# Kernel optimization log

Hardware: AMD Instinct MI355X
Metric: run time of the kernel (lower is better)

Reference implementation:

```python
import jax, jax.numpy as jnp
import numpy as np

N, E = 50000, 800000
HID, HEADS, HD = 128, 4, 32
EDIM, EGD = 16, 32


def _ln(x, g, b):
    mu = jnp.mean(x, axis=-1, keepdims=True)
    var = jnp.mean((x - mu) ** 2, axis=-1, keepdims=True)
    return (x - mu) / jnp.sqrt(var + 1e-5) * g + b


def _gelu(z):
    return jax.nn.gelu(z, approximate=False)


def setup_inputs() -> dict:
    key = jax.random.key(0)
    ks = jax.random.split(key, 16)
    n = lambda k, shape, s=1.0: jax.random.normal(k, shape, dtype=jnp.float32) * s
    return {
        "x": n(ks[0], (N, HID)),
        "edge_index": jax.random.randint(ks[1], (2, E), 0, N, dtype=jnp.int32),
        "edge_attr": n(ks[2], (E, EDIM)),
        "gamma": jax.random.uniform(ks[3], (N, HID), dtype=jnp.float32),
        "beta": n(ks[4], (N, HID), 0.1),
        "ln1_g": jnp.ones((HID,), jnp.float32), "ln1_b": jnp.zeros((HID,), jnp.float32),
        "Wq": n(ks[5], (HID, HEADS * HD), 0.05),
        "Wk": n(ks[6], (HID, HEADS * HD), 0.05),
        "Wv": n(ks[7], (HID, HEADS * HD), 0.05),
        "Wo": n(ks[8], (HEADS * HD, HID), 0.05), "bo": jnp.zeros((HID,), jnp.float32),
        "Wea1": n(ks[9], (EDIM, EGD), 0.1), "bea1": jnp.zeros((EGD,), jnp.float32),
        "Wea2": n(ks[10], (EGD, HEADS), 0.1), "bea2": jnp.zeros((HEADS,), jnp.float32),
        "Weg1": n(ks[11], (EDIM, EGD), 0.1), "beg1": jnp.zeros((EGD,), jnp.float32),
        "Weg2": n(ks[12], (EGD, HEADS * HD), 0.1), "beg2": jnp.zeros((HEADS * HD,), jnp.float32),
        "ln2_g": jnp.ones((HID,), jnp.float32), "ln2_b": jnp.zeros((HID,), jnp.float32),
        "Wf1": n(ks[13], (HID, 2 * HID), 0.05), "bf1": jnp.zeros((2 * HID,), jnp.float32),
        "Wf2": n(ks[14], (2 * HID, HID), 0.05), "bf2": jnp.zeros((HID,), jnp.float32),
    }


def reference(x, edge_index, edge_attr, gamma, beta,
              ln1_g, ln1_b, Wq, Wk, Wv, Wo, bo,
              Wea1, bea1, Wea2, bea2, Weg1, beg1, Weg2, beg2,
              ln2_g, ln2_b, Wf1, bf1, Wf2, bf2):
    n_nodes = x.shape[0]
    src, dst = edge_index[0], edge_index[1]
    scale = HD ** -0.5

    x_n = _ln(x, ln1_g, ln1_b)
    Q = (x_n @ Wq).reshape(n_nodes, HEADS, HD)
    K = (x_n @ Wk).reshape(n_nodes, HEADS, HD)
    V = (x_n @ Wv).reshape(n_nodes, HEADS, HD)

    # per-edge attention logits, edge-bias modulated  [E, h]
    logits = jnp.einsum('ehd,ehd->eh', Q[dst], K[src]) * scale
    logits = logits + (_gelu(edge_attr @ Wea1 + bea1) @ Wea2 + bea2)

    # sparse softmax over destination neighbourhoods (torch scatter_reduce amax
    # includes the zero-initialised accumulator -> max with 0)
    m = jax.ops.segment_max(logits, dst, num_segments=n_nodes)
    m = jnp.maximum(m, 0.0)
    el = jnp.exp(logits - m[dst])
    s = jax.ops.segment_sum(el, dst, num_segments=n_nodes)
    attn = el / (s[dst] + 1e-10)                      # [E, h]

    # per-edge sigmoid gate on values  [E, h, d]
    e_gate = jax.nn.sigmoid(_gelu(edge_attr @ Weg1 + beg1) @ Weg2 + beg2)
    weighted = attn[:, :, None] * (e_gate.reshape(-1, HEADS, HD) * V[src])
    out = jax.ops.segment_sum(weighted, dst, num_segments=n_nodes)
    out = out.reshape(n_nodes, HEADS * HD) @ Wo + bo

    out = gamma * out + beta                          # FiLM (dropout=0, eval)
    x = x + out
    x = x + (_gelu(_ln(x, ln2_g, ln2_b) @ Wf1 + bf1) @ Wf2 + bf2)
    return x
```

## Files before the change

### kernel.cpp

```cpp
#include <hip/hip_runtime.h>
#include <cmath>

#define N_NODES 50000
#define E_EDGES 800000
#define HID 128
#define HEADS 4
#define EDIM 16
#define EGD 32
#define VSTRIDE 136
#define SCAN_BS 512
#define SCAN_NB ((N_NODES + SCAN_BS - 1) / SCAN_BS)

typedef __attribute__((ext_vector_type(8))) short bf16x8;
typedef __attribute__((ext_vector_type(4))) float f32x4;

__device__ __forceinline__ float erf_fast(float x) {
    const float ax = fabsf(x);
    const float t = __builtin_amdgcn_rcpf(fmaf(0.3275911f, ax, 1.0f));
    float p = fmaf(1.061405429f, t, -1.453152027f);
    p = fmaf(p, t, 1.421413741f);
    p = fmaf(p, t, -0.284496736f);
    p = fmaf(p, t, 0.254829592f);
    p = p * t;
    const float e = __expf(-ax * ax);
    const float r = fmaf(-p, e, 1.0f);
    return copysignf(r, x);
}
__device__ __forceinline__ float gelu_f(float z) {
    return 0.5f * z * (1.0f + erf_fast(z * 0.7071067811865476f));
}
__device__ __forceinline__ float sigmoid_fast(float z) {
    return __builtin_amdgcn_rcpf(1.0f + __expf(-z));
}
__device__ __forceinline__ short f2bf(float f) {
    unsigned u = __float_as_uint(f);
    unsigned r = u + 0x7fffu + ((u >> 16) & 1u);
    return (short)(r >> 16);
}
__device__ __forceinline__ float bf2f(unsigned short u) {
    return __uint_as_float(((unsigned)u) << 16);
}

__global__ void __launch_bounds__(256) k0w_conv(
    const float* __restrict__ Wq, const float* __restrict__ Wk, const float* __restrict__ Wv,
    const float* __restrict__ Wo, const float* __restrict__ Wf1, const float* __restrict__ Wf2,
    const float* __restrict__ Wea1, const float* __restrict__ Wea2,
    const float* __restrict__ Weg1, const float* __restrict__ Weg2,
    unsigned short* __restrict__ Wqm, unsigned short* __restrict__ Wkm,
    unsigned short* __restrict__ Wvm, unsigned short* __restrict__ Wom,
    unsigned short* __restrict__ Wf1m, unsigned short* __restrict__ Wf2m,
    unsigned short* __restrict__ Wea1m, unsigned short* __restrict__ Wea2m,
    unsigned short* __restrict__ Wg1m, unsigned short* __restrict__ Wg2m)
{
    const int b = blockIdx.x, t = threadIdx.x;
    if (b == 512) {
        for (int i = t; i < 1024; i += 256) {
            const int j = i & 7, rest = i >> 3;
            const int n = rest & 31, q = rest >> 5, k = q * 8 + j;
            Wea1m[i] = (unsigned short)((k < EDIM) ? f2bf(Wea1[k * EGD + n]) : (short)0);
        }
        for (int i = t; i < 512; i += 256) {
            const int j = i & 7, rest = i >> 3;
            const int n = rest & 15, q = rest >> 4, k = q * 8 + j;
            Wea2m[i] = (unsigned short)((n < HEADS) ? f2bf(Wea2[k * HEADS + n]) : (short)0);
        }
        for (int i = t; i < 1024; i += 256) {
            const int j = i & 7, rest = i >> 3;
            const int c15 = rest & 15, qn = rest >> 4;
            const int q = qn >> 1, n = qn & 1;
            const int k = q * 8 + j;
            Wg1m[i] = (unsigned short)((k < EDIM) ? f2bf(Weg1[k * EGD + n * 16 + c15]) : (short)0);
        }
        for (int i = t; i < 4096; i += 256) {
            const int j = i & 7, rest = i >> 3;
            const int c15 = rest & 15, rest2 = rest >> 4;
            const int tt = rest2 & 7, q = rest2 >> 3;
            const int k = q * 8 + j;
            Wg2m[i] = (unsigned short)f2bf(Weg2[k * HID + tt * 16 + c15]);
        }
        return;
    }
    const float* src; unsigned short* dst; int idx; bool wide;
    if (b < 64)       { src = Wq;  dst = Wqm;  idx = b * 256 + t;         wide = false; }
    else if (b < 128) { src = Wk;  dst = Wkm;  idx = (b - 64) * 256 + t;  wide = false; }
    else if (b < 192) { src = Wv;  dst = Wvm;  idx = (b - 128) * 256 + t; wide = false; }
    else if (b < 256) { src = Wo;  dst = Wom;  idx = (b - 192) * 256 + t; wide = false; }
    else if (b < 384) { src = Wf1; dst = Wf1m; idx = (b - 256) * 256 + t; wide = true;  }
    else              { src = Wf2; dst = Wf2m; idx = (b - 384) * 256 + t; wide = false; }
    int k, n, N;
    if (wide) { k = idx >> 8; n = idx & 255; N = 256; }
    else      { k = idx >> 7; n = idx & 127; N = 128; }
    dst[((size_t)(k >> 3) * N + n) * 8 + (k & 7)] = (unsigned short)f2bf(src[idx]);
}

__global__ void __launch_bounds__(256) k1_ln_qkv(
    const float* __restrict__ x, const float* __restrict__ g1, const float* __restrict__ b1,
    const unsigned short* __restrict__ Wqm, const unsigned short* __restrict__ Wkm,
    const unsigned short* __restrict__ Wvm,
    unsigned short* __restrict__ Qb, unsigned short* __restrict__ Kb,
    unsigned short* __restrict__ Vb)
{
    __shared__ float xsm[16][HID];
    __shared__ __align__(16) unsigned short xnb[16 * HID];
    const int t = threadIdx.x;
    const int base = blockIdx.x * 16;
    {
        const float4* src = (const float4*)(x + (size_t)base * HID);
        float4* dst = (float4*)xsm;
        dst[t] = src[t];
        dst[t + 256] = src[t + 256];
    }
    __syncthreads();
    {
        const int sr = t >> 4, sl = t & 15;
        float s1 = 0.f, s2 = 0.f, v[8];
        #pragma unroll
        for (int j = 0; j < 8; ++j) { v[j] = xsm[sr][sl + 16 * j]; s1 += v[j]; s2 += v[j] * v[j]; }
        #pragma unroll
        for (int m = 1; m < 16; m <<= 1) { s1 += __shfl_xor(s1, m); s2 += __shfl_xor(s2, m); }
        const float mu = s1 * (1.0f / HID);
        const float rstd = rsqrtf(s2 * (1.0f / HID) - mu * mu + 1e-5f);
        char* rowp = (char*)(xnb + sr * HID);
        #pragma unroll
        for (int j = 0; j < 8; ++j) {
            const int col = sl + 16 * j;
            const float nv = (v[j] - mu) * rstd * g1[col] + b1[col];
            *(unsigned short*)(rowp + ((col * 2) ^ ((sr & 7) << 4))) = (unsigned short)f2bf(nv);
        }
    }
    __syncthreads();
    const int w = t >> 6, l = t & 63, q = l >> 4, c15 = l & 15;
    bf16x8 a[4];
    {
        const char* rowp = (const char*)(xnb + c15 * HID);
        #pragma unroll
        for (int kc = 0; kc < 4; ++kc)
            a[kc] = *(const bf16x8*)(rowp + ((kc * 64 + q * 16) ^ ((c15 & 7) << 4)));
    }
    const f32x4 zc = {0.f, 0.f, 0.f, 0.f};
    #pragma unroll
    for (int ct = 0; ct < 2; ++ct) {
        const int colb = (w * 2 + ct) * 16;
        f32x4 aq = zc, ak = zc, av = zc;
        #pragma unroll
        for (int kc = 0; kc < 4; ++kc) {
            const size_t boff = (size_t)((kc * 4 + q) * HID + colb + c15) * 8;
            aq = __builtin_amdgcn_mfma_f32_16x16x32_bf16(a[kc], *(const bf16x8*)(Wqm + boff), aq, 0, 0, 0);
            ak = __builtin_amdgcn_mfma_f32_16x16x32_bf16(a[kc], *(const bf16x8*)(Wkm + boff), ak, 0, 0, 0);
            av = __builtin_amdgcn_mfma_f32_16x16x32_bf16(a[kc], *(const bf16x8*)(Wvm + boff), av, 0, 0, 0);
        }
        #pragma unroll
        for (int r = 0; r < 4; ++r) {
            const size_t idx = (size_t)(base + q * 4 + r) * HID + colb + c15;
            Qb[idx] = (unsigned short)f2bf(aq[r]);
            Kb[idx] = (unsigned short)f2bf(ak[r]);
            Vb[idx] = (unsigned short)f2bf(av[r]);
        }
    }
}

__global__ void __launch_bounds__(256) k0a_degree(
    const int* __restrict__ ei, int* __restrict__ deg)
{
    const int e = blockIdx.x * 256 + threadIdx.x;
    atomicAdd(deg + ei[E_EDGES + e], 1);
}

__global__ void __launch_bounds__(SCAN_BS) k0b_scan1(
    const int* __restrict__ deg, int* __restrict__ rowptr, int* __restrict__ bsum)
{
    __shared__ int sm[SCAN_BS];
    const int t = threadIdx.x;
    const int i = blockIdx.x * SCAN_BS + t;
    const int v = (i < N_NODES) ? deg[i] : 0;
    sm[t] = v;
    __syncthreads();
    #pragma unroll
    for (int off = 1; off < SCAN_BS; off <<= 1) {
        int add = (t >= off) ? sm[t - off] : 0;
        __syncthreads();
        sm[t] += add;
        __syncthreads();
    }
    if (i < N_NODES) rowptr[i] = sm[t] - v;
    if (t == SCAN_BS - 1) bsum[blockIdx.x] = sm[t];
}

__global__ void __launch_bounds__(128) k0c_scan2(int* __restrict__ bsum)
{
    __shared__ int sm[128];
    const int t = threadIdx.x;
    const int v = (t < SCAN_NB) ? bsum[t] : 0;
    sm[t] = v;
    __syncthreads();
    #pragma unroll
    for (int off = 1; off < 128; off <<= 1) {
        int add = (t >= off) ? sm[t - off] : 0;
        __syncthreads();
        sm[t] += add;
        __syncthreads();
    }
    if (t < SCAN_NB) bsum[t] = sm[t] - v;
}

__global__ void __launch_bounds__(SCAN_BS) k0d_fixup(
    int* __restrict__ rowptr, int* __restrict__ wptr, const int* __restrict__ bsum)
{
    const int i = blockIdx.x * SCAN_BS + threadIdx.x;
    if (i < N_NODES) {
        int r = rowptr[i] + bsum[blockIdx.x];
        rowptr[i] = r;
        wptr[i] = r;
    }
    if (i == 0) rowptr[N_NODES] = E_EDGES;
}

__global__ void __launch_bounds__(256) k0e_scatter(
    const int* __restrict__ ei, int* __restrict__ wptr,
    int* __restrict__ eidx, int* __restrict__ esrc, int* __restrict__ pdst)
{
    const int e = blockIdx.x * 256 + threadIdx.x;
    const int d = ei[E_EDGES + e];
    const int pos = atomicAdd(wptr + d, 1);
    eidx[pos] = e;
    esrc[pos] = ei[e];
    pdst[pos] = d;
}

__global__ void __launch_bounds__(256) k2_fused(
    const int* __restrict__ eidx, const int* __restrict__ esrc, const int* __restrict__ pdst,
    const unsigned short* __restrict__ Qb, const unsigned short* __restrict__ Kb,
    const float* __restrict__ ea,
    const unsigned short* __restrict__ Wea1m, const float* __restrict__ bea1,
    const unsigned short* __restrict__ Wea2m, const float* __restrict__ bea2,
    float* __restrict__ logits,
    unsigned short* __restrict__ eab)
{
    __shared__ __align__(16) float dot_lds[4][16][4];
    __shared__ __align__(16) short h_lds[4][16 * EGD];
    const int t = threadIdx.x;
    const int w = t >> 6, l = t & 63;
    const int p0 = blockIdx.x * 64 + w * 16;

    {
        const int er = l >> 4;
        const int i = l & 15;
        const int head = i >> 2, part = i & 3;
        #pragma unroll
        for (int cc = 0; cc < 4; ++cc) {
            const int p = p0 + cc * 4 + er;
            const int dst = pdst[p], src = esrc[p];
            const bf16x8 qv = *(const bf16x8*)(Qb + (size_t)dst * HID + head * 32 + part * 8);
            const bf16x8 kv = *(const bf16x8*)(Kb + (size_t)src * HID + head * 32 + part * 8);
            float s = 0.f;
            #pragma unroll
            for (int j = 0; j < 8; ++j)
                s = fmaf(bf2f((unsigned short)qv[j]), bf2f((unsigned short)kv[j]), s);
            s += __shfl_xor(s, 1);
            s += __shfl_xor(s, 2);
            if (part == 0) dot_lds[w][cc * 4 + er][head] = s * 0.17677669529663689f;
        }
    }

    const int q = l >> 4, c15 = l & 15;
    bf16x8 a1 = {0, 0, 0, 0, 0, 0, 0, 0};
    if (q < 2) {
        const int e = eidx[p0 + c15];
        const float4 u0 = *(const float4*)(ea + (size_t)e * EDIM + q * 8);
        const float4 u1 = *(const float4*)(ea + (size_t)e * EDIM + q * 8 + 4);
        a1[0] = f2bf(u0.x); a1[1] = f2bf(u0.y); a1[2] = f2bf(u0.z); a1[3] = f2bf(u0.w);
        a1[4] = f2bf(u1.x); a1[5] = f2bf(u1.y); a1[6] = f2bf(u1.z); a1[7] = f2bf(u1.w);
        *(bf16x8*)(eab + (size_t)(p0 + c15) * EDIM + q * 8) = a1;
    }
    const bf16x8 b1f0 = *(const bf16x8*)(Wea1m + (size_t)(q * 32 + c15) * 8);
    const bf16x8 b1f1 = *(const bf16x8*)(Wea1m + (size_t)(q * 32 + 16 + c15) * 8);
    const f32x4 zc = {0.f, 0.f, 0.f, 0.f};
    f32x4 c0 = __builtin_amdgcn_mfma_f32_16x16x32_bf16(a1, b1f0, zc, 0, 0, 0);
    f32x4 c1 = __builtin_amdgcn_mfma_f32_16x16x32_bf16(a1, b1f1, zc, 0, 0, 0);
    const float bb0 = bea1[c15], bb1 = bea1[16 + c15];
    #pragma unroll
    for (int r = 0; r < 4; ++r) {
        h_lds[w][(q * 4 + r) * EGD + c15]      = f2bf(gelu_f(c0[r] + bb0));
        h_lds[w][(q * 4 + r) * EGD + 16 + c15] = f2bf(gelu_f(c1[r] + bb1));
    }
    asm volatile("s_waitcnt lgkmcnt(0)" ::: "memory");
    __builtin_amdgcn_sched_barrier(0);
    const bf16x8 a2 = *(const bf16x8*)&h_lds[w][c15 * EGD + q * 8];
    const bf16x8 b2 = *(const bf16x8*)(Wea2m + (size_t)(q * 16 + c15) * 8);
    f32x4 d2 = __builtin_amdgcn_mfma_f32_16x16x32_bf16(a2, b2, zc, 0, 0, 0);
    if (c15 < 4) {
        const float be = bea2[c15];
        #pragma unroll
        for (int r = 0; r < 4; ++r) {
            const int edge = q * 4 + r;
            const int p = p0 + edge;
            logits[(size_t)p * 4 + c15] = dot_lds[w][edge][c15] + d2[r] + be;
        }
    }
}

__global__ void __launch_bounds__(256, 8) k4_mfma(
    const int* __restrict__ rowptr, const int* __restrict__ esrc,
    const unsigned short* __restrict__ eab,
    const unsigned short* __restrict__ Wg1m, const float* __restrict__ beg1,
    const unsigned short* __restrict__ Wg2m, const float* __restrict__ beg2,
    const float* __restrict__ logits,
    const unsigned short* __restrict__ Vb, unsigned short* __restrict__ aggb)
{
    __shared__ __align__(16) short h_lds[4][16 * EGD];
    __shared__ __align__(16) float attn_lds[4][16][4];
    __shared__ __align__(16) unsigned short vsm[4][16 * VSTRIDE];
    const int t = threadIdx.x;
    const int wid = t >> 6, l = t & 63;
    const int q = l >> 4, c15 = l & 15;

    const float b1c0 = beg1[c15], b1c1 = beg1[16 + c15];
    float bg2[8];
    #pragma unroll
    for (int tt = 0; tt < 8; ++tt) bg2[tt] = beg2[tt * 16 + c15];

    const f32x4 zc = {0.f, 0.f, 0.f, 0.f};
    const int n = blockIdx.x * 4 + wid;
    const int pstart = rowptr[n], pend = rowptr[n + 1];

    const int pidx = pstart + l;
    const int my_src = (pidx < pend) ? esrc[pidx] : 0;

    const int slot = l >> 2, head = l & 3;
    float ssum = 0.f, el0 = 0.f;
    for (int pc = pstart; pc < pend; pc += 16) {
        const int cnt = min(16, pend - pc);
        float el = 0.f;
        if (slot < cnt) el = __expf(logits[(size_t)(pc + slot) * 4 + head]);
        if (pc == pstart) el0 = el;
        ssum += el;
    }
    ssum += __shfl_xor(ssum, 4);
    ssum += __shfl_xor(ssum, 8);
    ssum += __shfl_xor(ssum, 16);
    ssum += __shfl_xor(ssum, 32);
    const float invh = __builtin_amdgcn_rcpf(ssum + 1e-10f);

    float accv[8];
    #pragma unroll
    for (int tt = 0; tt < 8; ++tt) accv[tt] = 0.f;

    const int srow = l >> 2;
    const int ssub = l & 3;

    for (int pc = pstart; pc < pend; pc += 16) {
        const int cnt = min(16, pend - pc);
        const int sidx = (srow < cnt) ? srow : cnt - 1;
        const int rel = pc - pstart + sidx;
        const int srcrow = (rel < 64) ? __shfl(my_src, rel) : esrc[pc + sidx];
        bf16x8 vreg[4];
        #pragma unroll
        for (int i = 0; i < 4; ++i)
            vreg[i] = *(const bf16x8*)(Vb + (size_t)srcrow * HID + ssub * 32 + i * 8);
        const float el = (pc == pstart) ? el0
            : ((slot < cnt) ? __expf(logits[(size_t)(pc + slot) * 4 + head]) : 0.f);
        attn_lds[wid][slot][head] = el * invh;
        bf16x8 a1 = {0, 0, 0, 0, 0, 0, 0, 0};
        if (q < 2 && c15 < cnt)
            a1 = *(const bf16x8*)(eab + (size_t)(pc + c15) * EDIM + q * 8);
        const bf16x8 b1f0 = *(const bf16x8*)(Wg1m + (size_t)((q * 2 + 0) * 16 + c15) * 8);
        const bf16x8 b1f1 = *(const bf16x8*)(Wg1m + (size_t)((q * 2 + 1) * 16 + c15) * 8);
        f32x4 c0 = __builtin_amdgcn_mfma_f32_16x16x32_bf16(a1, b1f0, zc, 0, 0, 0);
        f32x4 c1 = __builtin_amdgcn_mfma_f32_16x16x32_bf16(a1, b1f1, zc, 0, 0, 0);
        #pragma unroll
        for (int r = 0; r < 4; ++r) {
            h_lds[wid][(q * 4 + r) * EGD + c15]      = f2bf(gelu_f(c0[r] + b1c0));
            h_lds[wid][(q * 4 + r) * EGD + 16 + c15] = f2bf(gelu_f(c1[r] + b1c1));
        }
        #pragma unroll
        for (int i = 0; i < 4; ++i)
            *(bf16x8*)&vsm[wid][srow * VSTRIDE + ssub * 32 + i * 8] = vreg[i];
        asm volatile("s_waitcnt lgkmcnt(0)" ::: "memory");
        __builtin_amdgcn_sched_barrier(0);
        const bf16x8 a2 = *(const bf16x8*)&h_lds[wid][c15 * EGD + q * 8];
        f32x4 at[4];
        #pragma unroll
        for (int r = 0; r < 4; ++r)
            at[r] = *(const f32x4*)&attn_lds[wid][q * 4 + r][0];
        f32x4 g[8];
        #pragma unroll
        for (int tt = 0; tt < 8; ++tt) {
            const bf16x8 b2 = *(const bf16x8*)(Wg2m + (size_t)((q * 8 + tt) * 16 + c15) * 8);
            g[tt] = __builtin_amdgcn_mfma_f32_16x16x32_bf16(a2, b2, zc, 0, 0, 0);
        }
        #pragma unroll
        for (int tt = 0; tt < 8; ++tt) {
            #pragma unroll
            for (int r = 0; r < 4; ++r) {
                const float sg = sigmoid_fast(g[tt][r] + bg2[tt]);
                const float aw = (tt < 2) ? at[r][0] : (tt < 4) ? at[r][1]
                               : (tt < 6) ? at[r][2] : at[r][3];
                const float vv = bf2f(vsm[wid][(q * 4 + r) * VSTRIDE + tt * 16 + c15]);
                accv[tt] = fmaf(aw * sg, vv, accv[tt]);
            }
        }
    }
    #pragma unroll
    for (int tt = 0; tt < 8; ++tt) {
        accv[tt] += __shfl_xor(accv[tt], 16);
        accv[tt] += __shfl_xor(accv[tt], 32);
    }
    aggb[(size_t)n * HID + (2 * q) * 16 + c15]     = (unsigned short)f2bf(accv[2 * q]);
    aggb[(size_t)n * HID + (2 * q + 1) * 16 + c15] = (unsigned short)f2bf(accv[2 * q + 1]);
}

__global__ void __launch_bounds__(256) k5_out(
    const unsigned short* __restrict__ aggb, const unsigned short* __restrict__ Wom,
    const float* __restrict__ bo,
    const float* __restrict__ gamma, const float* __restrict__ beta,
    const float* __restrict__ x,
    const float* __restrict__ g2, const float* __restrict__ b2,
    const unsigned short* __restrict__ Wf1m, const float* __restrict__ bf1,
    const unsigned short* __restrict__ Wf2m, const float* __restrict__ bf2,
    float* __restrict__ out)
{
    __shared__ float xlsm[16][HID];
    __shared__ __align__(16) unsigned short xnb[16 * HID];
    __shared__ __align__(16) unsigned short hb[16 * 2 * HID];
    const int t = threadIdx.x;
    const int base = blockIdx.x * 16;
    const int w = t >> 6, l = t & 63, q = l >> 4, c15 = l & 15;
    const f32x4 zc = {0.f, 0.f, 0.f, 0.f};

    bf16x8 a[4];
    #pragma unroll
    for (int kc = 0; kc < 4; ++kc)
        a[kc] = *(const bf16x8*)(aggb + (size_t)(base + c15) * HID + kc * 32 + q * 8);
    float xl[2][4];
    #pragma unroll
    for (int ct = 0; ct < 2; ++ct) {
        const int colb = (w * 2 + ct) * 16;
        f32x4 acc = zc;
        #pragma unroll
        for (int kc = 0; kc < 4; ++kc)
            acc = __builtin_amdgcn_mfma_f32_16x16x32_bf16(
                a[kc], *(const bf16x8*)(Wom + (size_t)((kc * 4 + q) * HID + colb + c15) * 8), acc, 0, 0, 0);
        const float bov = bo[colb + c15];
        #pragma unroll
        for (int r = 0; r < 4; ++r) {
            const int row = q * 4 + r;
            const size_t idx = (size_t)(base + row) * HID + colb + c15;
            float o = acc[r] + bov;
            o = fmaf(gamma[idx], o, beta[idx]);
            const float v = x[idx] + o;
            xl[ct][r] = v;
            xlsm[row][colb + c15] = v;
        }
    }
    __syncthreads();
    {
        const int sr = t >> 4, sl = t & 15;
        float s1 = 0.f, s2 = 0.f, v[8];
        #pragma unroll
        for (int j = 0; j < 8; ++j) { v[j] = xlsm[sr][sl + 16 * j]; s1 += v[j]; s2 += v[j] * v[j]; }
        #pragma unroll
        for (int m = 1; m < 16; m <<= 1) { s1 += __shfl_xor(s1, m); s2 += __shfl_xor(s2, m); }
        const float mu = s1 * (1.0f / HID);
        const float rstd = rsqrtf(s2 * (1.0f / HID) - mu * mu + 1e-5f);
        char* rowp = (char*)(xnb + sr * HID);
        #pragma unroll
        for (int j = 0; j < 8; ++j) {
            const int col = sl + 16 * j;
            const float nv = (v[j] - mu) * rstd * g2[col] + b2[col];
            *(unsigned short*)(rowp + ((col * 2) ^ ((sr & 7) << 4))) = (unsigned short)f2bf(nv);
        }
    }
    __syncthreads();
    {
        const char* rowp = (const char*)(xnb + c15 * HID);
        bf16x8 a2[4];
        #pragma unroll
        for (int kc = 0; kc < 4; ++kc)
            a2[kc] = *(const bf16x8*)(rowp + ((kc * 64 + q * 16) ^ ((c15 & 7) << 4)));
        #pragma unroll
        for (int ct = 0; ct < 4; ++ct) {
            const int colb = (w * 4 + ct) * 16;
            f32x4 acc = zc;
            #pragma unroll
            for (int kc = 0; kc < 4; ++kc)
                acc = __builtin_amdgcn_mfma_f32_16x16x32_bf16(
                    a2[kc], *(const bf16x8*)(Wf1m + (size_t)((kc * 4 + q) * 256 + colb + c15) * 8), acc, 0, 0, 0);
            const float b1v = bf1[colb + c15];
            #pragma unroll
            for (int r = 0; r < 4; ++r) {
                const int row = q * 4 + r;
                const float hg = gelu_f(acc[r] + b1v);
                *(unsigned short*)((char*)(hb + row * 2 * HID)
                    + (((colb + c15) * 2) ^ ((row & 7) << 4))) = (unsigned short)f2bf(hg);
            }
        }
    }
    __syncthreads();
    {
        const char* rowp = (const char*)(hb + c15 * 2 * HID);
        bf16x8 a3[8];
        #pragma unroll
        for (int kc = 0; kc < 8; ++kc)
            a3[kc] = *(const bf16x8*)(rowp + ((kc * 64 + q * 16) ^ ((c15 & 7) << 4)));
        #pragma unroll
        for (int ct = 0; ct < 2; ++ct) {
            const int colb = (w * 2 + ct) * 16;
            f32x4 acc = zc;
            #pragma unroll
            for (int kc = 0; kc < 8; ++kc)
                acc = __builtin_amdgcn_mfma_f32_16x16x32_bf16(
                    a3[kc], *(const bf16x8*)(Wf2m + (size_t)((kc * 4 + q) * HID + colb + c15) * 8), acc, 0, 0, 0);
            const float b2v = bf2[colb + c15];
            #pragma unroll
            for (int r = 0; r < 4; ++r) {
                const int row = q * 4 + r;
                out[(size_t)(base + row) * HID + colb + c15] = xl[ct][r] + acc[r] + b2v;
            }
        }
    }
}

extern "C" void kernel_launch(void* const* d_in, const int* in_sizes, int n_in,
                              void* d_out, int out_size, void* d_ws, size_t ws_size,
                              hipStream_t stream) {
    const float* x     = (const float*)d_in[0];
    const int*   ei    = (const int*)d_in[1];
    const float* ea    = (const float*)d_in[2];
    const float* gamma = (const float*)d_in[3];
    const float* beta  = (const float*)d_in[4];
    const float* ln1_g = (const float*)d_in[5];
    const float* ln1_b = (const float*)d_in[6];
    const float* Wq    = (const float*)d_in[7];
    const float* Wk    = (const float*)d_in[8];
    const float* Wv    = (const float*)d_in[9];
    const float* Wo    = (const float*)d_in[10];
    const float* bo    = (const float*)d_in[11];
    const float* Wea1  = (const float*)d_in[12];
    const float* bea1  = (const float*)d_in[13];
    const float* Wea2  = (const float*)d_in[14];
    const float* bea2  = (const float*)d_in[15];
    const float* Weg1  = (const float*)d_in[16];
    const float* beg1  = (const float*)d_in[17];
    const float* Weg2  = (const float*)d_in[18];
    const float* beg2  = (const float*)d_in[19];
    const float* ln2_g = (const float*)d_in[20];
    const float* ln2_b = (const float*)d_in[21];
    const float* Wf1   = (const float*)d_in[22];
    const float* bf1   = (const float*)d_in[23];
    const float* Wf2   = (const float*)d_in[24];
    const float* bf2   = (const float*)d_in[25];

    unsigned short* Qb   = (unsigned short*)d_ws;
    unsigned short* Kb   = Qb + (size_t)N_NODES * HID;
    unsigned short* Vb   = Kb + (size_t)N_NODES * HID;
    unsigned short* aggb = Vb + (size_t)N_NODES * HID;
    unsigned short* eab  = aggb + (size_t)N_NODES * HID;
    unsigned short* Wqm  = eab + (size_t)E_EDGES * EDIM;
    unsigned short* Wkm  = Wqm + 16384;
    unsigned short* Wvm  = Wkm + 16384;
    unsigned short* Wom  = Wvm + 16384;
    unsigned short* Wf1m = Wom + 16384;
    unsigned short* Wf2m = Wf1m + 32768;
    unsigned short* Wea1m = Wf2m + 32768;
    unsigned short* Wea2m = Wea1m + 1024;
    unsigned short* Wg1m  = Wea2m + 512;
    unsigned short* Wg2m  = Wg1m + 1024;
    float* logits = (float*)(Wg2m + 4096);
    int*   deg    = (int*)(logits + (size_t)E_EDGES * 4);
    int*   rowptr = deg + N_NODES;
    int*   wptr   = rowptr + (N_NODES + 1);
    int*   bsum   = wptr + N_NODES;
    int*   eidx   = bsum + 128;
    int*   esrc   = eidx + E_EDGES;
    int*   pdst   = esrc + E_EDGES;

    hipMemsetAsync(deg, 0, (size_t)N_NODES * sizeof(int), stream);

    k0w_conv<<<513, 256, 0, stream>>>(Wq, Wk, Wv, Wo, Wf1, Wf2, Wea1, Wea2, Weg1, Weg2,
                                      Wqm, Wkm, Wvm, Wom, Wf1m, Wf2m, Wea1m, Wea2m,
                                      Wg1m, Wg2m);

    k0a_degree<<<E_EDGES / 256, 256, 0, stream>>>(ei, deg);
    k0b_scan1<<<SCAN_NB, SCAN_BS, 0, stream>>>(deg, rowptr, bsum);
    k0c_scan2<<<1, 128, 0, stream>>>(bsum);
    k0d_fixup<<<SCAN_NB, SCAN_BS, 0, stream>>>(rowptr, wptr, bsum);
    k0e_scatter<<<E_EDGES / 256, 256, 0, stream>>>(ei, wptr, eidx, esrc, pdst);

    k1_ln_qkv<<<N_NODES / 16, 256, 0, stream>>>(x, ln1_g, ln1_b, Wqm, Wkm, Wvm,
                                                Qb, Kb, Vb);
    k2_fused<<<E_EDGES / 64, 256, 0, stream>>>(eidx, esrc, pdst, Qb, Kb, ea,
                                               Wea1m, bea1, Wea2m, bea2,
                                               logits, eab);
    k4_mfma<<<N_NODES / 4, 256, 0, stream>>>(rowptr, esrc, eab,
                                             Wg1m, beg1, Wg2m, beg2,
                                             logits, Vb, aggb);
    k5_out<<<N_NODES / 16, 256, 0, stream>>>(aggb, Wom, bo, gamma, beta, x,
                                             ln2_g, ln2_b, Wf1m, bf1, Wf2m, bf2,
                                             (float*)d_out);
}
```

Measured before the change: 336.9 us.

## Pack CSR edge arrays into int4 and defer softmax normalization to single pass

The three separate CSR arrays (edge id, source, destination) are packed into one int4 record per edge, so the scatter writes and later reads touch one 16-byte element instead of three scattered ints. The aggregation kernel drops its separate first pass that computed softmax denominators. It now accumulates unnormalized exp-weighted values in a single pass and divides by the per-head sum at the end, which removes a re-read of logits and one exp evaluation per edge. The cost is wider per-edge records (the fourth int is padding), and the sum is applied per output head after the reduction.

After: 347.0 us. +3.0%, slower.

```diff
diff --git a/kernel.cpp b/kernel.cpp
--- a/kernel.cpp
+++ b/kernel.cpp
@@ -216,19 +216,17 @@
 }
 
 __global__ void __launch_bounds__(256) k0e_scatter(
-    const int* __restrict__ ei, int* __restrict__ wptr,
-    int* __restrict__ eidx, int* __restrict__ esrc, int* __restrict__ pdst)
+    const int* __restrict__ ei, int* __restrict__ wptr, int4* __restrict__ edata)
 {
     const int e = blockIdx.x * 256 + threadIdx.x;
+    const int s = ei[e];
     const int d = ei[E_EDGES + e];
     const int pos = atomicAdd(wptr + d, 1);
-    eidx[pos] = e;
-    esrc[pos] = ei[e];
-    pdst[pos] = d;
+    edata[pos] = make_int4(e, s, d, 0);
 }
 
 __global__ void __launch_bounds__(256) k2_fused(
-    const int* __restrict__ eidx, const int* __restrict__ esrc, const int* __restrict__ pdst,
+    const int4* __restrict__ edata,
     const unsigned short* __restrict__ Qb, const unsigned short* __restrict__ Kb,
     const float* __restrict__ ea,
     const unsigned short* __restrict__ Wea1m, const float* __restrict__ bea1,
@@ -249,9 +247,9 @@
         #pragma unroll
         for (int cc = 0; cc < 4; ++cc) {
             const int p = p0 + cc * 4 + er;
-            const int dst = pdst[p], src = esrc[p];
-            const bf16x8 qv = *(const bf16x8*)(Qb + (size_t)dst * HID + head * 32 + part * 8);
-            const bf16x8 kv = *(const bf16x8*)(Kb + (size_t)src * HID + head * 32 + part * 8);
+            const int4 ed = edata[p];
+            const bf16x8 qv = *(const bf16x8*)(Qb + (size_t)ed.z * HID + head * 32 + part * 8);
+            const bf16x8 kv = *(const bf16x8*)(Kb + (size_t)ed.y * HID + head * 32 + part * 8);
             float s = 0.f;
             #pragma unroll
             for (int j = 0; j < 8; ++j)
@@ -265,7 +263,7 @@
     const int q = l >> 4, c15 = l & 15;
     bf16x8 a1 = {0, 0, 0, 0, 0, 0, 0, 0};
     if (q < 2) {
-        const int e = eidx[p0 + c15];
+        const int e = edata[p0 + c15].x;
         const float4 u0 = *(const float4*)(ea + (size_t)e * EDIM + q * 8);
         const float4 u1 = *(const float4*)(ea + (size_t)e * EDIM + q * 8 + 4);
         a1[0] = f2bf(u0.x); a1[1] = f2bf(u0.y); a1[2] = f2bf(u0.z); a1[3] = f2bf(u0.w);
@@ -300,7 +298,7 @@
 }
 
 __global__ void __launch_bounds__(256, 8) k4_mfma(
-    const int* __restrict__ rowptr, const int* __restrict__ esrc,
+    const int* __restrict__ rowptr, const int4* __restrict__ edata,
     const unsigned short* __restrict__ eab,
     const unsigned short* __restrict__ Wg1m, const float* __restrict__ beg1,
     const unsigned short* __restrict__ Wg2m, const float* __restrict__ beg2,
@@ -324,42 +322,26 @@
     const int pstart = rowptr[n], pend = rowptr[n + 1];
 
     const int pidx = pstart + l;
-    const int my_src = (pidx < pend) ? esrc[pidx] : 0;
+    const int my_src = (pidx < pend) ? edata[pidx].y : 0;
 
     const int slot = l >> 2, head = l & 3;
-    float ssum = 0.f, el0 = 0.f;
+    float ssum = 0.f;
+    float accv[8];
+    #pragma unroll
+    for (int tt = 0; tt < 8; ++tt) accv[tt] = 0.f;
+
     for (int pc = pstart; pc < pend; pc += 16) {
         const int cnt = min(16, pend - pc);
-        float el = 0.f;
-        if (slot < cnt) el = __expf(logits[(size_t)(pc + slot) * 4 + head]);
-        if (pc == pstart) el0 = el;
+        const int sidx = (slot < cnt) ? slot : cnt - 1;
+        const int rel = pc - pstart + sidx;
+        const int srcrow = (rel < 64) ? __shfl(my_src, rel) : edata[pc + sidx].y;
+        bf16x8 vreg[4];
+        #pragma unroll
+        for (int i = 0; i < 4; ++i)
+            vreg[i] = *(const bf16x8*)(Vb + (size_t)srcrow * HID + head * 32 + i * 8);
+        const float el = (slot < cnt) ? __expf(logits[(size_t)(pc + slot) * 4 + head]) : 0.f;
         ssum += el;
-    }
-    ssum += __shfl_xor(ssum, 4);
-    ssum += __shfl_xor(ssum, 8);
-    ssum += __shfl_xor(ssum, 16);
-    ssum += __shfl_xor(ssum, 32);
-    const float invh = __builtin_amdgcn_rcpf(ssum + 1e-10f);
-
-    float accv[8];
-    #pragma unroll
-    for (int tt = 0; tt < 8; ++tt) accv[tt] = 0.f;
-
-    const int srow = l >> 2;
-    const int ssub = l & 3;
-
-    for (int pc = pstart; pc < pend; pc += 16) {
-        const int cnt = min(16, pend - pc);
-        const int sidx = (srow < cnt) ? srow : cnt - 1;
-        const int rel = pc - pstart + sidx;
-        const int srcrow = (rel < 64) ? __shfl(my_src, rel) : esrc[pc + sidx];
-        bf16x8 vreg[4];
-        #pragma unroll
-        for (int i = 0; i < 4; ++i)
-            vreg[i] = *(const bf16x8*)(Vb + (size_t)srcrow * HID + ssub * 32 + i * 8);
-        const float el = (pc == pstart) ? el0
-            : ((slot < cnt) ? __expf(logits[(size_t)(pc + slot) * 4 + head]) : 0.f);
-        attn_lds[wid][slot][head] = el * invh;
+        attn_lds[wid][slot][head] = el;
         bf16x8 a1 = {0, 0, 0, 0, 0, 0, 0, 0};
         if (q < 2 && c15 < cnt)
             a1 = *(const bf16x8*)(eab + (size_t)(pc + c15) * EDIM + q * 8);
@@ -374,7 +356,7 @@
         }
         #pragma unroll
         for (int i = 0; i < 4; ++i)
-            *(bf16x8*)&vsm[wid][srow * VSTRIDE + ssub * 32 + i * 8] = vreg[i];
+            *(bf16x8*)&vsm[wid][slot * VSTRIDE + head * 32 + i * 8] = vreg[i];
         asm volatile("s_waitcnt lgkmcnt(0)" ::: "memory");
         __builtin_amdgcn_sched_barrier(0);
         const bf16x8 a2 = *(const bf16x8*)&h_lds[wid][c15 * EGD + q * 8];
@@ -400,13 +382,18 @@
             }
         }
     }
+    ssum += __shfl_xor(ssum, 4);
+    ssum += __shfl_xor(ssum, 8);
+    ssum += __shfl_xor(ssum, 16);
+    ssum += __shfl_xor(ssum, 32);
+    const float invq = __builtin_amdgcn_rcpf(__shfl(ssum, q) + 1e-10f);
     #pragma unroll
     for (int tt = 0; tt < 8; ++tt) {
         accv[tt] += __shfl_xor(accv[tt], 16);
         accv[tt] += __shfl_xor(accv[tt], 32);
     }
-    aggb[(size_t)n * HID + (2 * q) * 16 + c15]     = (unsigned short)f2bf(accv[2 * q]);
-    aggb[(size_t)n * HID + (2 * q + 1) * 16 + c15] = (unsigned short)f2bf(accv[2 * q + 1]);
+    aggb[(size_t)n * HID + (2 * q) * 16 + c15]     = (unsigned short)f2bf(accv[2 * q] * invq);
+    aggb[(size_t)n * HID + (2 * q + 1) * 16 + c15] = (unsigned short)f2bf(accv[2 * q + 1] * invq);
 }
 
 __global__ void __launch_bounds__(256) k5_out(
@@ -566,13 +553,11 @@
     unsigned short* Wg1m  = Wea2m + 512;
     unsigned short* Wg2m  = Wg1m + 1024;
     float* logits = (float*)(Wg2m + 4096);
-    int*   deg    = (int*)(logits + (size_t)E_EDGES * 4);
+    int4*  edata  = (int4*)(logits + (size_t)E_EDGES * 4);
+    int*   deg    = (int*)(edata + E_EDGES);
     int*   rowptr = deg + N_NODES;
     int*   wptr   = rowptr + (N_NODES + 1);
     int*   bsum   = wptr + N_NODES;
-    int*   eidx   = bsum + 128;
-    int*   esrc   = eidx + E_EDGES;
-    int*   pdst   = esrc + E_EDGES;
 
     hipMemsetAsync(deg, 0, (size_t)N_NODES * sizeof(int), stream);
 
@@ -584,14 +569,14 @@
     k0b_scan1<<<SCAN_NB, SCAN_BS, 0, stream>>>(deg, rowptr, bsum);
     k0c_scan2<<<1, 128, 0, stream>>>(bsum);
     k0d_fixup<<<SCAN_NB, SCAN_BS, 0, stream>>>(rowptr, wptr, bsum);
-    k0e_scatter<<<E_EDGES / 256, 256, 0, stream>>>(ei, wptr, eidx, esrc, pdst);
+    k0e_scatter<<<E_EDGES / 256, 256, 0, stream>>>(ei, wptr, edata);
 
     k1_ln_qkv<<<N_NODES / 16, 256, 0, stream>>>(x, ln1_g, ln1_b, Wqm, Wkm, Wvm,
                                                 Qb, Kb, Vb);
-    k2_fused<<<E_EDGES / 64, 256, 0, stream>>>(eidx, esrc, pdst, Qb, Kb, ea,
+    k2_fused<<<E_EDGES / 64, 256, 0, stream>>>(edata, Qb, Kb, ea,
                                                Wea1m, bea1, Wea2m, bea2,
                                                logits, eab);
-    k4_mfma<<<N_NODES / 4, 256, 0, stream>>>(rowptr, esrc, eab,
+    k4_mfma<<<N_NODES / 4, 256, 0, stream>>>(rowptr, edata, eab,
                                              Wg1m, beg1, Wg2m, beg2,
                                              logits, Vb, aggb);
     k5_out<<<N_NODES / 16, 256, 0, stream>>>(aggb, Wom, bo, gamma, beta, x,
```

## Fuse softmax normalization into single pass and use one-wave blocks in k4

Applied to the files above, without the earlier changes.

The aggregation kernel no longer makes a separate pass over logits to compute the softmax denominator. It accumulates unnormalized exp-weighted values together with the per-head sum, then multiplies by the reciprocal at the end. Logits and the gate weights and biases are pre-scaled by log2(e) so cheaper exp2 can replace exp. The kernel now launches one 64-thread wave per node instead of four waves per block, which cuts shared memory per block and may change occupancy and scheduling. Rounding changes slightly because normalization happens after accumulation and the log2(e) scaling is applied before the bf16 cast.

Measured after the change: 437.8 us. 29.9% more time.

```diff
diff --git a/kernel.cpp b/kernel.cpp
--- a/kernel.cpp
+++ b/kernel.cpp
@@ -8,6 +8,7 @@
 #define EDIM 16
 #define EGD 32
 #define VSTRIDE 136
+#define LOG2E 1.4426950408889634f
 #define SCAN_BS 512
 #define SCAN_NB ((N_NODES + SCAN_BS - 1) / SCAN_BS)
 
@@ -29,9 +30,6 @@
 __device__ __forceinline__ float gelu_f(float z) {
     return 0.5f * z * (1.0f + erf_fast(z * 0.7071067811865476f));
 }
-__device__ __forceinline__ float sigmoid_fast(float z) {
-    return __builtin_amdgcn_rcpf(1.0f + __expf(-z));
-}
 __device__ __forceinline__ short f2bf(float f) {
     unsigned u = __float_as_uint(f);
     unsigned r = u + 0x7fffu + ((u >> 16) & 1u);
@@ -76,7 +74,7 @@
             const int c15 = rest & 15, rest2 = rest >> 4;
             const int tt = rest2 & 7, q = rest2 >> 3;
             const int k = q * 8 + j;
-            Wg2m[i] = (unsigned short)f2bf(Weg2[k * HID + tt * 16 + c15]);
+            Wg2m[i] = (unsigned short)f2bf(Weg2[k * HID + tt * 16 + c15] * LOG2E);
         }
         return;
     }
@@ -294,12 +292,12 @@
         for (int r = 0; r < 4; ++r) {
             const int edge = q * 4 + r;
             const int p = p0 + edge;
-            logits[(size_t)p * 4 + c15] = dot_lds[w][edge][c15] + d2[r] + be;
-        }
-    }
-}
-
-__global__ void __launch_bounds__(256, 8) k4_mfma(
+            logits[(size_t)p * 4 + c15] = (dot_lds[w][edge][c15] + d2[r] + be) * LOG2E;
+        }
+    }
+}
+
+__global__ void __launch_bounds__(64, 8) k4_mfma(
     const int* __restrict__ rowptr, const int* __restrict__ esrc,
     const unsigned short* __restrict__ eab,
     const unsigned short* __restrict__ Wg1m, const float* __restrict__ beg1,
@@ -307,59 +305,42 @@
     const float* __restrict__ logits,
     const unsigned short* __restrict__ Vb, unsigned short* __restrict__ aggb)
 {
-    __shared__ __align__(16) short h_lds[4][16 * EGD];
-    __shared__ __align__(16) float attn_lds[4][16][4];
-    __shared__ __align__(16) unsigned short vsm[4][16 * VSTRIDE];
-    const int t = threadIdx.x;
-    const int wid = t >> 6, l = t & 63;
+    __shared__ __align__(16) short h_lds[16 * EGD];
+    __shared__ __align__(16) float attn_lds[16][4];
+    __shared__ __align__(16) unsigned short vsm[16 * VSTRIDE];
+    const int l = threadIdx.x;
     const int q = l >> 4, c15 = l & 15;
 
     const float b1c0 = beg1[c15], b1c1 = beg1[16 + c15];
     float bg2[8];
     #pragma unroll
-    for (int tt = 0; tt < 8; ++tt) bg2[tt] = beg2[tt * 16 + c15];
+    for (int tt = 0; tt < 8; ++tt) bg2[tt] = beg2[tt * 16 + c15] * LOG2E;
 
     const f32x4 zc = {0.f, 0.f, 0.f, 0.f};
-    const int n = blockIdx.x * 4 + wid;
+    const int n = blockIdx.x;
     const int pstart = rowptr[n], pend = rowptr[n + 1];
 
     const int pidx = pstart + l;
     const int my_src = (pidx < pend) ? esrc[pidx] : 0;
 
     const int slot = l >> 2, head = l & 3;
-    float ssum = 0.f, el0 = 0.f;
+    float ssum = 0.f;
+    float accv[8];
+    #pragma unroll
+    for (int tt = 0; tt < 8; ++tt) accv[tt] = 0.f;
+
     for (int pc = pstart; pc < pend; pc += 16) {
         const int cnt = min(16, pend - pc);
-        float el = 0.f;
-        if (slot < cnt) el = __expf(logits[(size_t)(pc + slot) * 4 + head]);
-        if (pc == pstart) el0 = el;
-        ssum += el;
-    }
-    ssum += __shfl_xor(ssum, 4);
-    ssum += __shfl_xor(ssum, 8);
-    ssum += __shfl_xor(ssum, 16);
-    ssum += __shfl_xor(ssum, 32);
-    const float invh = __builtin_amdgcn_rcpf(ssum + 1e-10f);
-
-    float accv[8];
-    #pragma unroll
-    for (int tt = 0; tt < 8; ++tt) accv[tt] = 0.f;
-
-    const int srow = l >> 2;
-    const int ssub = l & 3;
-
-    for (int pc = pstart; pc < pend; pc += 16) {
-        const int cnt = min(16, pend - pc);
-        const int sidx = (srow < cnt) ? srow : cnt - 1;
+        const int sidx = (slot < cnt) ? slot : cnt - 1;
         const int rel = pc - pstart + sidx;
         const int srcrow = (rel < 64) ? __shfl(my_src, rel) : esrc[pc + sidx];
         bf16x8 vreg[4];
         #pragma unroll
         for (int i = 0; i < 4; ++i)
-            vreg[i] = *(const bf16x8*)(Vb + (size_t)srcrow * HID + ssub * 32 + i * 8);
-        const float el = (pc == pstart) ? el0
-            : ((slot < cnt) ? __expf(logits[(size_t)(pc + slot) * 4 + head]) : 0.f);
-        attn_lds[wid][slot][head] = el * invh;
+            vreg[i] = *(const bf16x8*)(Vb + (size_t)srcrow * HID + head * 32 + i * 8);
+        const float el = (slot < cnt) ? exp2f(logits[(size_t)(pc + slot) * 4 + head]) : 0.f;
+        ssum += el;
+        attn_lds[slot][head] = el;
         bf16x8 a1 = {0, 0, 0, 0, 0, 0, 0, 0};
         if (q < 2 && c15 < cnt)
             a1 = *(const bf16x8*)(eab + (size_t)(pc + c15) * EDIM + q * 8);
@@ -369,19 +350,19 @@
         f32x4 c1 = __builtin_amdgcn_mfma_f32_16x16x32_bf16(a1, b1f1, zc, 0, 0, 0);
         #pragma unroll
         for (int r = 0; r < 4; ++r) {
-            h_lds[wid][(q * 4 + r) * EGD + c15]      = f2bf(gelu_f(c0[r] + b1c0));
-            h_lds[wid][(q * 4 + r) * EGD + 16 + c15] = f2bf(gelu_f(c1[r] + b1c1));
+            h_lds[(q * 4 + r) * EGD + c15]      = f2bf(gelu_f(c0[r] + b1c0));
+            h_lds[(q * 4 + r) * EGD + 16 + c15] = f2bf(gelu_f(c1[r] + b1c1));
         }
         #pragma unroll
         for (int i = 0; i < 4; ++i)
-            *(bf16x8*)&vsm[wid][srow * VSTRIDE + ssub * 32 + i * 8] = vreg[i];
+            *(bf16x8*)&vsm[slot * VSTRIDE + head * 32 + i * 8] = vreg[i];
         asm volatile("s_waitcnt lgkmcnt(0)" ::: "memory");
         __builtin_amdgcn_sched_barrier(0);
-        const bf16x8 a2 = *(const bf16x8*)&h_lds[wid][c15 * EGD + q * 8];
+        const bf16x8 a2 = *(const bf16x8*)&h_lds[c15 * EGD + q * 8];
         f32x4 at[4];
         #pragma unroll
         for (int r = 0; r < 4; ++r)
-            at[r] = *(const f32x4*)&attn_lds[wid][q * 4 + r][0];
+            at[r] = *(const f32x4*)&attn_lds[q * 4 + r][0];
         f32x4 g[8];
         #pragma unroll
         for (int tt = 0; tt < 8; ++tt) {
@@ -392,21 +373,26 @@
         for (int tt = 0; tt < 8; ++tt) {
             #pragma unroll
             for (int r = 0; r < 4; ++r) {
-                const float sg = sigmoid_fast(g[tt][r] + bg2[tt]);
+                const float sg = __builtin_amdgcn_rcpf(1.0f + exp2f(-(g[tt][r] + bg2[tt])));
                 const float aw = (tt < 2) ? at[r][0] : (tt < 4) ? at[r][1]
                                : (tt < 6) ? at[r][2] : at[r][3];
-                const float vv = bf2f(vsm[wid][(q * 4 + r) * VSTRIDE + tt * 16 + c15]);
+                const float vv = bf2f(vsm[(q * 4 + r) * VSTRIDE + tt * 16 + c15]);
                 accv[tt] = fmaf(aw * sg, vv, accv[tt]);
             }
         }
     }
+    ssum += __shfl_xor(ssum, 4);
+    ssum += __shfl_xor(ssum, 8);
+    ssum += __shfl_xor(ssum, 16);
+    ssum += __shfl_xor(ssum, 32);
+    const float invq = __builtin_amdgcn_rcpf(__shfl(ssum, q) + 1e-10f);
     #pragma unroll
     for (int tt = 0; tt < 8; ++tt) {
         accv[tt] += __shfl_xor(accv[tt], 16);
         accv[tt] += __shfl_xor(accv[tt], 32);
     }
-    aggb[(size_t)n * HID + (2 * q) * 16 + c15]     = (unsigned short)f2bf(accv[2 * q]);
-    aggb[(size_t)n * HID + (2 * q + 1) * 16 + c15] = (unsigned short)f2bf(accv[2 * q + 1]);
+    aggb[(size_t)n * HID + (2 * q) * 16 + c15]     = (unsigned short)f2bf(accv[2 * q] * invq);
+    aggb[(size_t)n * HID + (2 * q + 1) * 16 + c15] = (unsigned short)f2bf(accv[2 * q + 1] * invq);
 }
 
 __global__ void __launch_bounds__(256) k5_out(
@@ -591,9 +577,9 @@
     k2_fused<<<E_EDGES / 64, 256, 0, stream>>>(eidx, esrc, pdst, Qb, Kb, ea,
                                                Wea1m, bea1, Wea2m, bea2,
                                                logits, eab);
-    k4_mfma<<<N_NODES / 4, 256, 0, stream>>>(rowptr, esrc, eab,
-                                             Wg1m, beg1, Wg2m, beg2,
-                                             logits, Vb, aggb);
+    k4_mfma<<<N_NODES, 64, 0, stream>>>(rowptr, esrc, eab,
+                                        Wg1m, beg1, Wg2m, beg2,
+                                        logits, Vb, aggb);
     k5_out<<<N_NODES / 16, 256, 0, stream>>>(aggb, Wom, bo, gamma, beta, x,
                                              ln2_g, ln2_b, Wf1m, bf1, Wf2m, bf2,
                                              (float*)d_out);
```
